# Kernel tuning notes

Measured on AMD Instinct MI355X. Metric: run time of the kernel, lower is better.

The kernel has to match this reference:

```python
import jax, jax.numpy as jnp
import numpy as np

B, S, D, H, F, NL, V = 4, 2048, 512, 8, 2048, 4, 32000
DH = D // H
EPS = 1e-6
LN_EPS = 1e-5


def _xavier(k, shape):
    lim = (6.0 / (shape[-2] + shape[-1])) ** 0.5
    return jax.random.uniform(k, shape, jnp.float32, -lim, lim)


def setup_inputs() -> dict:
    key = jax.random.key(0)
    ks = jax.random.split(key, 12)
    x = jax.random.randint(ks[0], (B, S), 0, V)
    emb = jax.random.normal(ks[1], (V, D), jnp.float32) * 0.02
    # sinusoidal positional encoding
    pos = np.arange(S, dtype=np.float32)[:, None]
    div = np.exp(np.arange(0, D, 2, dtype=np.float32) * (-np.log(10000.0) / D))
    pe_np = np.zeros((S, D), np.float32)
    pe_np[:, 0::2] = np.sin(pos * div)
    pe_np[:, 1::2] = np.cos(pos * div)
    pe = jnp.asarray(pe_np)
    return {
        "x": x, "emb": emb, "pe": pe,
        "Wq": _xavier(ks[2], (NL, D, D)), "bq": jnp.zeros((NL, D)),
        "Wk": _xavier(ks[3], (NL, D, D)), "bk": jnp.zeros((NL, D)),
        "Wv": _xavier(ks[4], (NL, D, D)), "bv": jnp.zeros((NL, D)),
        "Wo": _xavier(ks[5], (NL, D, D)), "bo": jnp.zeros((NL, D)),
        "W1": _xavier(ks[6], (NL, D, F)), "b1": jnp.zeros((NL, F)),
        "W2": _xavier(ks[7], (NL, F, D)), "b2": jnp.zeros((NL, D)),
        "g1": jnp.ones((NL, D)), "be1": jnp.zeros((NL, D)),
        "g2": jnp.ones((NL, D)), "be2": jnp.zeros((NL, D)),
        "gf": jnp.ones((D,)), "bf": jnp.zeros((D,)),
    }


def _layer_norm(h, g, b):
    mu = jnp.mean(h, axis=-1, keepdims=True)
    var = jnp.mean((h - mu) ** 2, axis=-1, keepdims=True)
    return (h - mu) * jax.lax.rsqrt(var + LN_EPS) * g + b


def _phi(u):
    # elu(x) + 1 feature map of fast-transformers causal-linear attention
    return jax.nn.elu(u) + 1.0


def _causal_linear_attention(q, k, v, key_mask):
    # q, k, v: [B, S, H, DH]; key_mask: [B, S] (1 for valid keys)
    Q = _phi(q)
    K = _phi(k) * key_mask[:, :, None, None]
    # cumulative state sum_{j<=i} K_j outer V_j : [B, S, H, DH, DH]
    St = jnp.cumsum(K[..., :, None] * v[..., None, :], axis=1)
    num = jnp.einsum("bshd,bshde->bshe", Q, St)
    Z = 1.0 / (jnp.einsum("bshd,bshd->bsh", Q, jnp.cumsum(K, axis=1)) + EPS)
    return num * Z[..., None]


def reference(x, emb, pe, Wq, bq, Wk, bk, Wv, bv, Wo, bo,
              W1, b1, W2, b2, g1, be1, g2, be2, gf, bf):
    # length mask from nonzero token count (LengthMask semantics)
    lengths = jnp.sum(jnp.abs(x) != 0, axis=-1)  # [B]
    key_mask = (jnp.arange(S)[None, :] < lengths[:, None]).astype(jnp.float32)
    h = emb[x] + pe[None, :, :]  # [B, S, D]
    for i in range(NL):
        q = (h @ Wq[i] + bq[i]).reshape(B, S, H, DH)
        k = (h @ Wk[i] + bk[i]).reshape(B, S, H, DH)
        v = (h @ Wv[i] + bv[i]).reshape(B, S, H, DH)
        a = _causal_linear_attention(q, k, v, key_mask).reshape(B, S, D)
        a = a @ Wo[i] + bo[i]
        h = _layer_norm(h + a, g1[i], be1[i])
        y = jax.nn.relu(h @ W1[i] + b1[i]) @ W2[i] + b2[i]
        h = _layer_norm(h + y, g2[i], be2[i])
    return _layer_norm(h, gf, bf)
```

## Files before the change

kernel.cpp:

```cpp
#include <hip/hip_runtime.h>
#include <math.h>

#define NLAYER 4
#define BB 4
#define SS 2048
#define DD 512
#define HH 8
#define DH 64
#define FF 2048
#define TT (BB*SS)
#define LCH 64
#define NCH (SS/LCH)
#define LN_EPS 1e-5f
#define ATT_EPS 1e-6f

typedef __bf16 bf16x8 __attribute__((ext_vector_type(8)));
typedef float  f32x4  __attribute__((ext_vector_type(4)));
typedef float  f32x16 __attribute__((ext_vector_type(16)));

__device__ __forceinline__ unsigned short f2bf(float f) {
    union { float f; unsigned u; } a; a.f = f;
    unsigned u = a.u;
    unsigned r = (u + 0x7FFFu + ((u >> 16) & 1u)) >> 16;
    return (unsigned short)r;
}
__device__ __forceinline__ float bf2f(unsigned short s) {
    union { unsigned u; float f; } a; a.u = ((unsigned)s) << 16;
    return a.f;
}
__device__ __forceinline__ float phi_f(float u) {
    return u > 0.f ? u + 1.f : __expf(u);
}

__global__ __launch_bounds__(64)
void len_kernel(const int* __restrict__ x, int* __restrict__ len) {
    const int b = blockIdx.x;
    int cnt = 0;
    for (int s = threadIdx.x; s < SS; s += 64) cnt += (x[b * SS + s] != 0);
    #pragma unroll
    for (int off = 32; off; off >>= 1) cnt += __shfl_xor(cnt, off);
    if (threadIdx.x == 0) len[b] = cnt;
}

__global__ __launch_bounds__(256)
void embed_kernel(const int* __restrict__ x, const float* __restrict__ emb,
                  const float* __restrict__ pe, unsigned short* __restrict__ h) {
    int t = blockIdx.x * 256 + threadIdx.x;
    int row = t >> 6, q = t & 63;
    int tok = x[row];
    int s = row & (SS - 1);
    const float4* ep = (const float4*)(emb + (size_t)tok * DD);
    const float4* pp = (const float4*)(pe + (size_t)s * DD);
    float4 e0 = ep[q * 2], e1 = ep[q * 2 + 1];
    float4 p0 = pp[q * 2], p1 = pp[q * 2 + 1];
    ushort4 u0 = make_ushort4(f2bf(e0.x + p0.x), f2bf(e0.y + p0.y),
                              f2bf(e0.z + p0.z), f2bf(e0.w + p0.w));
    ushort4 u1 = make_ushort4(f2bf(e1.x + p1.x), f2bf(e1.y + p1.y),
                              f2bf(e1.z + p1.z), f2bf(e1.w + p1.w));
    size_t base = (size_t)row * DD + q * 8;
    *(ushort4*)(h + base) = u0;
    *(ushort4*)(h + base + 4) = u1;
}

__global__ __launch_bounds__(256)
void transpose_cvt(const float* __restrict__ src, unsigned short* __restrict__ dst,
                   int R, int C, size_t srcLS, size_t dstLS) {
    __shared__ float tile[32][33];
    const int z = blockIdx.z;
    src += (size_t)z * srcLS;
    dst += (size_t)z * dstLS;
    const int c0 = blockIdx.x * 32, r0 = blockIdx.y * 32;
    const int tx = threadIdx.x & 31, ty = threadIdx.x >> 5;
    #pragma unroll
    for (int i = 0; i < 32; i += 8)
        tile[ty + i][tx] = src[(size_t)(r0 + ty + i) * C + c0 + tx];
    __syncthreads();
    #pragma unroll
    for (int i = 0; i < 32; i += 8)
        dst[(size_t)(c0 + ty + i) * R + r0 + tx] = f2bf(tile[tx][ty + i]);
}

__global__ __launch_bounds__(256)
void bias_concat(const float* __restrict__ bq, const float* __restrict__ bk,
                 const float* __restrict__ bv, float* __restrict__ bqkv) {
    int idx = blockIdx.x * 256 + threadIdx.x;
    if (idx >= NLAYER * 1536) return;
    int l = idx / 1536, n = idx % 1536;
    float v = n < 512 ? bq[l * 512 + n] : (n < 1024 ? bk[l * 512 + n - 512] : bv[l * 512 + n - 1024]);
    bqkv[idx] = v;
}

__device__ __forceinline__ void gll16(void* lds_ptr, const void* g_ptr) {
    __builtin_amdgcn_global_load_lds(
        (const __attribute__((address_space(1))) void*)g_ptr,
        (__attribute__((address_space(3))) void*)lds_ptr, 16, 0, 0);
}

template<int RELU, int WB>
__global__ __launch_bounds__(256, 2)
void gemm_bt(const unsigned short* __restrict__ A, const unsigned short* __restrict__ Bt,
             const float* __restrict__ bias, float* __restrict__ Cf,
             unsigned short* __restrict__ Cb, int M, int N, int K) {
    __shared__ __align__(16) char lds[2 * 2 * 128 * 64 * 2];
    const int Nt = N >> 7;
    const int bid = blockIdx.x;
    const int swz = (bid & 7) * ((int)gridDim.x >> 3) + (bid >> 3);
    const int m0 = (swz / Nt) * 128;
    const int n0 = (swz % Nt) * 128;
    const int tid = threadIdx.x;
    const int w = tid >> 6, lane = tid & 63;
    const int wr = w >> 1, wc = w & 1;
    const int srow = lane >> 3, scc = lane & 7;
    const int l32 = lane & 31, khalf = lane >> 5;

    f32x16 acc[2][2] = {};

    auto stage = [&](int buf, int k0) {
        char* base = lds + buf * 32768;
        #pragma unroll
        for (int op = 0; op < 2; ++op) {
            const unsigned short* G = op ? Bt : A;
            const int r0 = op ? n0 : m0;
            char* obase = base + op * 16384;
            #pragma unroll
            for (int i = 0; i < 4; ++i) {
                int ii = w * 4 + i;
                int row = ii * 8 + srow;
                int chunk = scc ^ (row & 7);
                gll16(obase + ii * 1024,
                      G + (size_t)(r0 + row) * K + k0 + chunk * 8);
            }
        }
    };

    stage(0, 0);
    const int nt = K >> 6;
    int buf = 0;
    const int rA = wr * 64 + l32;
    const int rB = wc * 64 + l32;

    for (int kt = 0; kt < nt; ++kt) {
        __syncthreads();
        if (kt + 1 < nt) stage(buf ^ 1, (kt + 1) << 6);
        const char* pA = lds + buf * 32768;
        const char* pB = pA + 16384;
        bf16x8 af[2][4], bfr[2][4];
        #pragma unroll
        for (int mf = 0; mf < 2; ++mf)
            #pragma unroll
            for (int kk = 0; kk < 4; ++kk) {
                int row = rA + mf * 32;
                int c = (kk * 2 + khalf) ^ (row & 7);
                af[mf][kk] = *(const bf16x8*)(pA + row * 128 + c * 16);
            }
        #pragma unroll
        for (int nf = 0; nf < 2; ++nf)
            #pragma unroll
            for (int kk = 0; kk < 4; ++kk) {
                int row = rB + nf * 32;
                int c = (kk * 2 + khalf) ^ (row & 7);
                bfr[nf][kk] = *(const bf16x8*)(pB + row * 128 + c * 16);
            }
        #pragma unroll
        for (int kk = 0; kk < 4; ++kk)
            #pragma unroll
            for (int mf = 0; mf < 2; ++mf)
                #pragma unroll
                for (int nf = 0; nf < 2; ++nf)
                    acc[mf][nf] = __builtin_amdgcn_mfma_f32_32x32x16_bf16(
                        af[mf][kk], bfr[nf][kk], acc[mf][nf], 0, 0, 0);
        buf ^= 1;
    }

    #pragma unroll
    for (int nf = 0; nf < 2; ++nf) {
        int col = n0 + wc * 64 + nf * 32 + l32;
        float bi = bias[col];
        #pragma unroll
        for (int mf = 0; mf < 2; ++mf) {
            int rowb = m0 + wr * 64 + mf * 32 + 4 * khalf;
            #pragma unroll
            for (int reg = 0; reg < 16; ++reg) {
                int row = rowb + (reg & 3) + 8 * (reg >> 2);
                float v = acc[mf][nf][reg] + bi;
                if (RELU) v = v > 0.f ? v : 0.f;
                if (WB) Cb[(size_t)row * N + col] = f2bf(v);
                else    Cf[(size_t)row * N + col] = v;
            }
        }
    }
}

template<int RELU>
__global__ __launch_bounds__(512, 2)
void gemm_big(const unsigned short* __restrict__ A, const unsigned short* __restrict__ Bt,
              const float* __restrict__ bias, unsigned short* __restrict__ Cb,
              int M, int N, int K) {
    __shared__ __align__(16) char lds[3 * 49152];
    const int Nt = N >> 7;
    const int bid = blockIdx.x;
    const int swz = (bid & 7) * ((int)gridDim.x >> 3) + (bid >> 3);
    const int m0 = (swz / Nt) * 256;
    const int n0 = (swz % Nt) * 128;
    const int tid = threadIdx.x;
    const int w = tid >> 6, lane = tid & 63;
    const int wr = w >> 1, wc = w & 1;
    const int l32 = lane & 31, khalf = lane >> 5;

    f32x16 acc[2][2] = {};

    auto stage = [&](int buf, int k0) {
        char* base = lds + buf * 49152;
        #pragma unroll
        for (int s = 0; s < 4; ++s) {
            int lin0 = s * 512 + w * 64;
            int lin = lin0 + lane;
            int row = lin >> 3, chunk = lin & 7;
            gll16(base + lin0 * 16,
                  A + (size_t)(m0 + row) * K + k0 + ((chunk ^ (row & 7)) << 3));
        }
        #pragma unroll
        for (int s = 0; s < 2; ++s) {
            int lin0 = s * 512 + w * 64;
            int lin = lin0 + lane;
            int row = lin >> 3, chunk = lin & 7;
            gll16(base + 32768 + lin0 * 16,
                  Bt + (size_t)(n0 + row) * K + k0 + ((chunk ^ (row & 7)) << 3));
        }
    };

    const int nt = K >> 6;
    stage(0, 0);
    stage(1, 64);
    int cur = 0;
    const int rA = wr * 64 + l32;
    const int rB = wc * 64 + l32;

    for (int t = 0; t < nt; ++t) {
        asm volatile("s_waitcnt lgkmcnt(0)" ::: "memory");
        if (t + 1 < nt) asm volatile("s_waitcnt vmcnt(6)" ::: "memory");
        else            asm volatile("s_waitcnt vmcnt(0)" ::: "memory");
        __builtin_amdgcn_s_barrier();
        __builtin_amdgcn_sched_barrier(0);
        if (t + 2 < nt) {
            int nb = cur + 2; if (nb >= 3) nb -= 3;
            stage(nb, (t + 2) << 6);
        }
        const char* pA = lds + cur * 49152;
        const char* pB = pA + 32768;
        bf16x8 af[2][4], bfr[2][4];
        #pragma unroll
        for (int mf = 0; mf < 2; ++mf)
            #pragma unroll
            for (int kk = 0; kk < 4; ++kk) {
                int row = rA + mf * 32;
                int c = (kk * 2 + khalf) ^ (row & 7);
                af[mf][kk] = *(const bf16x8*)(pA + row * 128 + c * 16);
            }
        #pragma unroll
        for (int nf = 0; nf < 2; ++nf)
            #pragma unroll
            for (int kk = 0; kk < 4; ++kk) {
                int row = rB + nf * 32;
                int c = (kk * 2 + khalf) ^ (row & 7);
                bfr[nf][kk] = *(const bf16x8*)(pB + row * 128 + c * 16);
            }
        #pragma unroll
        for (int kk = 0; kk < 4; ++kk)
            #pragma unroll
            for (int mf = 0; mf < 2; ++mf)
                #pragma unroll
                for (int nf = 0; nf < 2; ++nf)
                    acc[mf][nf] = __builtin_amdgcn_mfma_f32_32x32x16_bf16(
                        af[mf][kk], bfr[nf][kk], acc[mf][nf], 0, 0, 0);
        cur = (cur + 1 == 3) ? 0 : cur + 1;
    }

    #pragma unroll
    for (int nf = 0; nf < 2; ++nf) {
        int col = n0 + wc * 64 + nf * 32 + l32;
        float bi = bias[col];
        #pragma unroll
        for (int mf = 0; mf < 2; ++mf) {
            int rowb = m0 + wr * 64 + mf * 32 + 4 * khalf;
            #pragma unroll
            for (int reg = 0; reg < 16; ++reg) {
                int row = rowb + (reg & 3) + 8 * (reg >> 2);
                float v = acc[mf][nf][reg] + bi;
                if (RELU) v = v > 0.f ? v : 0.f;
                Cb[(size_t)row * N + col] = f2bf(v);
            }
        }
    }
}

__global__ __launch_bounds__(256)
void attn_chunk_sums(const unsigned short* __restrict__ qkv, const int* __restrict__ len,
                     unsigned short* __restrict__ states, float* __restrict__ ksum) {
    const int c = blockIdx.x & (NCH - 1);
    const int bh = blockIdx.x / NCH;
    const int b = bh >> 3, h = bh & 7;
    const int L = len[b];
    const int tid = threadIdx.x;
    const int w = tid >> 6, lane = tid & 63;
    __shared__ __align__(16) unsigned short Kt[64 * 64];
    __shared__ __align__(16) unsigned short Vt[64 * 64];
    __shared__ float ksumP[4][64];

    float kpart = 0.f;
    #pragma unroll 8
    for (int t = 0; t < 16; ++t) {
        const int jj = 4 * t + w;
        const int d = lane;
        const int sglob = c * 64 + jj;
        const unsigned short* base = qkv + (size_t)(b * SS + sglob) * 1536 + h * 64 + d;
        float kv = bf2f(base[512]);
        float kp = (sglob < L) ? phi_f(kv) : 0.f;
        kpart += kp;
        const int sw = (((jj >> 3) ^ (d & 7)) << 3) + (jj & 7);
        Kt[d * 64 + sw] = f2bf(kp);
        Vt[d * 64 + sw] = base[1024];
    }
    ksumP[w][lane] = kpart;
    __syncthreads();

    const int frow = w * 16 + (lane & 15);
    const int g = lane >> 4;
    bf16x8 ak[2];
    #pragma unroll
    for (int kk = 0; kk < 2; ++kk)
        ak[kk] = *(const bf16x8*)&Kt[frow * 64 + (((kk * 4 + g) ^ (frow & 7)) << 3)];
    f32x4 oc[4] = {};
    #pragma unroll
    for (int ef = 0; ef < 4; ++ef) {
        int brow = ef * 16 + (lane & 15);
        #pragma unroll
        for (int kk = 0; kk < 2; ++kk) {
            bf16x8 bv = *(const bf16x8*)&Vt[brow * 64 + (((kk * 4 + g) ^ (brow & 7)) << 3)];
            oc[ef] = __builtin_amdgcn_mfma_f32_16x16x32_bf16(ak[kk], bv, oc[ef], 0, 0, 0);
        }
    }
    unsigned short* so = states + (size_t)blockIdx.x * 4096;
    #pragma unroll
    for (int ef = 0; ef < 4; ++ef)
        #pragma unroll
        for (int r = 0; r < 4; ++r) {
            int dd = w * 16 + g * 4 + r;
            int e = ef * 16 + (lane & 15);
            so[dd * 64 + e] = f2bf(oc[ef][r]);
        }
    if (w == 0) {
        float s = ksumP[0][lane] + ksumP[1][lane] + ksumP[2][lane] + ksumP[3][lane];
        ksum[(size_t)blockIdx.x * 64 + lane] = s;
    }
}

__global__ __launch_bounds__(256)
void attn_prefix(const unsigned short* __restrict__ states, const float* __restrict__ ksum,
                 unsigned short* __restrict__ sprefix, float* __restrict__ kprefix) {
    const int bh = blockIdx.x >> 4;
    const int idx = (blockIdx.x & 15) * 256 + threadIdx.x;
    size_t base = (size_t)bh * NCH * 4096 + idx;
    float run = 0.f;
    #pragma unroll 4
    for (int cc = 0; cc < NCH; ++cc) {
        size_t o = base + (size_t)cc * 4096;
        float v = bf2f(states[o]);
        sprefix[o] = f2bf(run);
        run += v;
    }
    if ((blockIdx.x & 15) == 0 && threadIdx.x < 64) {
        size_t kb = (size_t)bh * NCH * 64 + threadIdx.x;
        float krun = 0.f;
        for (int cc = 0; cc < NCH; ++cc) {
            size_t o = kb + (size_t)cc * 64;
            float v = ksum[o];
            kprefix[o] = krun;
            krun += v;
        }
    }
}

__global__ __launch_bounds__(256)
void attn_output(const unsigned short* __restrict__ qkv, const int* __restrict__ len,
                 const unsigned short* __restrict__ sprefix, const float* __restrict__ kprefix,
                 unsigned short* __restrict__ a_bf) {
    const int c = blockIdx.x & (NCH - 1);
    const int bh = blockIdx.x / NCH;
    const int b = bh >> 3, h = bh & 7;
    const int L = len[b];
    const int tid = threadIdx.x;
    const int w = tid >> 6, lane = tid & 63;

    __shared__ __align__(16) unsigned short Qb[64 * 64];
    __shared__ __align__(16) unsigned short Kb[64 * 64];
    __shared__ __align__(16) unsigned short SpT[64 * 64];
    __shared__ __align__(16) unsigned short Vt[64 * 64];
    __shared__ __align__(16) unsigned short Amb[64 * 64];
    __shared__ float zq[64];
    __shared__ float zinv[64];

    const float kspv = kprefix[(size_t)(bh * NCH + c) * 64 + lane];
    const unsigned short* Sp = sprefix + (size_t)(bh * NCH + c) * 4096;

    #pragma unroll 4
    for (int t = 0; t < 16; ++t) {
        const int jj = 4 * t + w;
        const int d = lane;
        const int sglob = c * 64 + jj;
        const unsigned short* base = qkv + (size_t)(b * SS + sglob) * 1536 + h * 64 + d;
        float qv = bf2f(base[0]), kv = bf2f(base[512]);
        float qp = phi_f(qv);
        float kp = (sglob < L) ? phi_f(kv) : 0.f;
        const int swr = (((d >> 3) ^ (jj & 7)) << 3) + (d & 7);
        Qb[jj * 64 + swr] = f2bf(qp);
        Kb[jj * 64 + swr] = f2bf(kp);
        const int swt = (((jj >> 3) ^ (d & 7)) << 3) + (jj & 7);
        Vt[d * 64 + swt] = base[1024];
        SpT[d * 64 + swt] = Sp[jj * 64 + d];
        float zc = qp * kspv;
        #pragma unroll
        for (int off = 32; off; off >>= 1) zc += __shfl_xor(zc, off);
        if (lane == 0) zq[jj] = zc;
    }
    __syncthreads();

    const int frow = w * 16 + (lane & 15);
    const int g = lane >> 4;
    bf16x8 aq[2];
    #pragma unroll
    for (int kk = 0; kk < 2; ++kk)
        aq[kk] = *(const bf16x8*)&Qb[frow * 64 + (((kk * 4 + g) ^ (frow & 7)) << 3)];

    f32x4 am[4] = {};
    #pragma unroll
    for (int jf = 0; jf < 4; ++jf) {
        int brow = jf * 16 + (lane & 15);
        #pragma unroll
        for (int kk = 0; kk < 2; ++kk) {
            bf16x8 bk = *(const bf16x8*)&Kb[brow * 64 + (((kk * 4 + g) ^ (brow & 7)) << 3)];
            am[jf] = __builtin_amdgcn_mfma_f32_16x16x32_bf16(aq[kk], bk, am[jf], 0, 0, 0);
        }
    }

    float zl[4] = {0.f, 0.f, 0.f, 0.f};
    #pragma unroll
    for (int jf = 0; jf < 4; ++jf) {
        #pragma unroll
        for (int r = 0; r < 4; ++r) {
            int i = w * 16 + g * 4 + r;
            int j = jf * 16 + (lane & 15);
            float v = (j <= i) ? am[jf][r] : 0.f;
            zl[r] += v;
            Amb[i * 64 + (((j >> 3) ^ (i & 7)) << 3) + (j & 7)] = f2bf(v);
        }
    }
    #pragma unroll
    for (int r = 0; r < 4; ++r)
        #pragma unroll
        for (int off = 1; off < 16; off <<= 1) zl[r] += __shfl_xor(zl[r], off);
    #pragma unroll
    for (int r = 0; r < 4; ++r) {
        if ((lane & 15) == r) {
            int i = w * 16 + g * 4 + r;
            zinv[i] = 1.f / (zl[r] + zq[i] + ATT_EPS);
        }
    }

    f32x4 oc[4] = {};
    #pragma unroll
    for (int ef = 0; ef < 4; ++ef) {
        int brow = ef * 16 + (lane & 15);
        #pragma unroll
        for (int kk = 0; kk < 2; ++kk) {
            bf16x8 bs = *(const bf16x8*)&SpT[brow * 64 + (((kk * 4 + g) ^ (brow & 7)) << 3)];
            oc[ef] = __builtin_amdgcn_mfma_f32_16x16x32_bf16(aq[kk], bs, oc[ef], 0, 0, 0);
        }
    }
    bf16x8 aam[2];
    #pragma unroll
    for (int kk = 0; kk < 2; ++kk)
        aam[kk] = *(const bf16x8*)&Amb[frow * 64 + (((kk * 4 + g) ^ (frow & 7)) << 3)];
    #pragma unroll
    for (int ef = 0; ef < 4; ++ef) {
        int brow = ef * 16 + (lane & 15);
        #pragma unroll
        for (int kk = 0; kk < 2; ++kk) {
            bf16x8 bv = *(const bf16x8*)&Vt[brow * 64 + (((kk * 4 + g) ^ (brow & 7)) << 3)];
            oc[ef] = __builtin_amdgcn_mfma_f32_16x16x32_bf16(aam[kk], bv, oc[ef], 0, 0, 0);
        }
    }

    __syncthreads();
    #pragma unroll
    for (int ef = 0; ef < 4; ++ef) {
        #pragma unroll
        for (int r = 0; r < 4; ++r) {
            int i = w * 16 + g * 4 + r;
            int e = ef * 16 + (lane & 15);
            float zi = zinv[i];
            Kb[i * 64 + (((e >> 3) ^ (i & 7)) << 3) + (e & 7)] = f2bf(oc[ef][r] * zi);
        }
    }
    __syncthreads();
    {
        unsigned short* dst = a_bf + (size_t)(b * SS + c * 64) * 512 + h * 64;
        #pragma unroll
        for (int u = 0; u < 2; ++u) {
            int cid = tid + u * 256;
            int row = cid >> 3, cb = cid & 7;
            int4 val = *(const int4*)&Kb[row * 64 + ((cb ^ (row & 7)) << 3)];
            *(int4*)(dst + (size_t)row * 512 + cb * 8) = val;
        }
    }
}

template<int ADD, int FINAL>
__global__ __launch_bounds__(256)
void ln_kernel(const unsigned short* __restrict__ hin, const unsigned short* __restrict__ add,
               const float* __restrict__ gw, const float* __restrict__ bw,
               unsigned short* __restrict__ hout, float* __restrict__ fout) {
    const int row = blockIdx.x * 4 + (threadIdx.x >> 6);
    const int lane = threadIdx.x & 63;
    const size_t base = (size_t)row * DD + lane * 8;
    float v[8];
    {
        ushort4 a0 = *(const ushort4*)(hin + base);
        ushort4 a1 = *(const ushort4*)(hin + base + 4);
        v[0] = bf2f(a0.x); v[1] = bf2f(a0.y); v[2] = bf2f(a0.z); v[3] = bf2f(a0.w);
        v[4] = bf2f(a1.x); v[5] = bf2f(a1.y); v[6] = bf2f(a1.z); v[7] = bf2f(a1.w);
    }
    if (ADD) {
        ushort4 b0 = *(const ushort4*)(add + base);
        ushort4 b1 = *(const ushort4*)(add + base + 4);
        v[0] += bf2f(b0.x); v[1] += bf2f(b0.y); v[2] += bf2f(b0.z); v[3] += bf2f(b0.w);
        v[4] += bf2f(b1.x); v[5] += bf2f(b1.y); v[6] += bf2f(b1.z); v[7] += bf2f(b1.w);
    }
    float s = 0.f;
    #pragma unroll
    for (int i = 0; i < 8; ++i) s += v[i];
    #pragma unroll
    for (int off = 32; off; off >>= 1) s += __shfl_xor(s, off);
    float mu = s * (1.f / 512.f);
    float sq = 0.f;
    #pragma unroll
    for (int i = 0; i < 8; ++i) { float d = v[i] - mu; sq += d * d; }
    #pragma unroll
    for (int off = 32; off; off >>= 1) sq += __shfl_xor(sq, off);
    float rs = 1.f / sqrtf(sq * (1.f / 512.f) + LN_EPS);
    float4 g0 = ((const float4*)gw)[lane * 2], g1v = ((const float4*)gw)[lane * 2 + 1];
    float4 b0 = ((const float4*)bw)[lane * 2], b1v = ((const float4*)bw)[lane * 2 + 1];
    float gg[8] = {g0.x, g0.y, g0.z, g0.w, g1v.x, g1v.y, g1v.z, g1v.w};
    float bb[8] = {b0.x, b0.y, b0.z, b0.w, b1v.x, b1v.y, b1v.z, b1v.w};
    float o[8];
    #pragma unroll
    for (int i = 0; i < 8; ++i) o[i] = (v[i] - mu) * rs * gg[i] + bb[i];
    if (FINAL) {
        *(float4*)(fout + base)     = make_float4(o[0], o[1], o[2], o[3]);
        *(float4*)(fout + base + 4) = make_float4(o[4], o[5], o[6], o[7]);
    } else {
        *(ushort4*)(hout + base)     = make_ushort4(f2bf(o[0]), f2bf(o[1]), f2bf(o[2]), f2bf(o[3]));
        *(ushort4*)(hout + base + 4) = make_ushort4(f2bf(o[4]), f2bf(o[5]), f2bf(o[6]), f2bf(o[7]));
    }
}

extern "C" void kernel_launch(void* const* d_in, const int* in_sizes, int n_in,
                              void* d_out, int out_size, void* d_ws, size_t ws_size,
                              hipStream_t stream) {
    (void)in_sizes; (void)n_in; (void)out_size; (void)ws_size;
    const int*   x   = (const int*)d_in[0];
    const float* emb = (const float*)d_in[1];
    const float* pe  = (const float*)d_in[2];
    const float* Wq  = (const float*)d_in[3];
    const float* bq  = (const float*)d_in[4];
    const float* Wk  = (const float*)d_in[5];
    const float* bk  = (const float*)d_in[6];
    const float* Wv  = (const float*)d_in[7];
    const float* bv  = (const float*)d_in[8];
    const float* Wo  = (const float*)d_in[9];
    const float* bo  = (const float*)d_in[10];
    const float* W1  = (const float*)d_in[11];
    const float* b1  = (const float*)d_in[12];
    const float* W2  = (const float*)d_in[13];
    const float* b2  = (const float*)d_in[14];
    const float* g1  = (const float*)d_in[15];
    const float* be1 = (const float*)d_in[16];
    const float* g2  = (const float*)d_in[17];
    const float* be2 = (const float*)d_in[18];
    const float* gf  = (const float*)d_in[19];
    const float* bff = (const float*)d_in[20];
    float* out = (float*)d_out;

    char* ws = (char*)d_ws;
    size_t off = 0;
    auto alloc = [&](size_t bytes) -> void* {
        void* p = ws + off; off += (bytes + 255) & ~(size_t)255; return p;
    };
    int* len              = (int*)alloc(16);
    unsigned short* qkv_t = (unsigned short*)alloc((size_t)NLAYER * 1536 * 512 * 2);
    unsigned short* wo_t  = (unsigned short*)alloc((size_t)NLAYER * 512 * 512 * 2);
    unsigned short* w1_t  = (unsigned short*)alloc((size_t)NLAYER * 2048 * 512 * 2);
    unsigned short* w2_t  = (unsigned short*)alloc((size_t)NLAYER * 512 * 2048 * 2);
    float* bqkv           = (float*)alloc((size_t)NLAYER * 1536 * 4);
    unsigned short* h     = (unsigned short*)alloc((size_t)TT * 512 * 2);
    unsigned short* qkv   = (unsigned short*)alloc((size_t)TT * 1536 * 2);
    unsigned short* a_bf  = (unsigned short*)alloc((size_t)TT * 512 * 2);
    unsigned short* obuf  = (unsigned short*)alloc((size_t)TT * 512 * 2);
    unsigned short* y1_bf = (unsigned short*)alloc((size_t)TT * 2048 * 2);
    unsigned short* states  = (unsigned short*)alloc((size_t)32 * NCH * 4096 * 2);
    float* ksum           = (float*)alloc((size_t)32 * NCH * 64 * 4);
    unsigned short* sprefix = (unsigned short*)alloc((size_t)32 * NCH * 4096 * 2);
    float* kprefix        = (float*)alloc((size_t)32 * NCH * 64 * 4);

    len_kernel<<<BB, 64, 0, stream>>>(x, len);
    embed_kernel<<<(TT * 64) / 256, 256, 0, stream>>>(x, emb, pe, h);

    dim3 tb(256);
    transpose_cvt<<<dim3(16, 16, NLAYER), tb, 0, stream>>>(Wq, qkv_t,             512, 512, (size_t)512*512, (size_t)1536*512);
    transpose_cvt<<<dim3(16, 16, NLAYER), tb, 0, stream>>>(Wk, qkv_t + 512*512,   512, 512, (size_t)512*512, (size_t)1536*512);
    transpose_cvt<<<dim3(16, 16, NLAYER), tb, 0, stream>>>(Wv, qkv_t + 1024*512,  512, 512, (size_t)512*512, (size_t)1536*512);
    transpose_cvt<<<dim3(16, 16, NLAYER), tb, 0, stream>>>(Wo, wo_t,              512, 512, (size_t)512*512, (size_t)512*512);
    transpose_cvt<<<dim3(64, 16, NLAYER), tb, 0, stream>>>(W1, w1_t,              512, 2048, (size_t)512*2048, (size_t)2048*512);
    transpose_cvt<<<dim3(16, 64, NLAYER), tb, 0, stream>>>(W2, w2_t,              2048, 512, (size_t)2048*512, (size_t)512*2048);
    bias_concat<<<(NLAYER * 1536 + 255) / 256, 256, 0, stream>>>(bq, bk, bv, bqkv);

    for (int l = 0; l < NLAYER; ++l) {
        gemm_big<0><<<(TT/256) * (1536/128), 512, 0, stream>>>(
            h, qkv_t + (size_t)l*1536*512, bqkv + l*1536, qkv, TT, 1536, 512);
        attn_chunk_sums<<<32 * NCH, 256, 0, stream>>>(qkv, len, states, ksum);
        attn_prefix<<<32 * 16, 256, 0, stream>>>(states, ksum, sprefix, kprefix);
        attn_output<<<32 * NCH, 256, 0, stream>>>(qkv, len, sprefix, kprefix, a_bf);
        gemm_bt<0,1><<<(TT/128) * (512/128), 256, 0, stream>>>(
            a_bf, wo_t + (size_t)l*512*512, bo + l*512, nullptr, obuf, TT, 512, 512);
        ln_kernel<1,0><<<TT/4, 256, 0, stream>>>(h, obuf, g1 + l*512, be1 + l*512, h, nullptr);
        gemm_big<1><<<(TT/256) * (2048/128), 512, 0, stream>>>(
            h, w1_t + (size_t)l*2048*512, b1 + l*2048, y1_bf, TT, 2048, 512);
        gemm_bt<0,1><<<(TT/128) * (512/128), 256, 0, stream>>>(
            y1_bf, w2_t + (size_t)l*512*2048, b2 + l*512, nullptr, obuf, TT, 512, 2048);
        ln_kernel<1,0><<<TT/4, 256, 0, stream>>>(h, obuf, g2 + l*512, be2 + l*512, h, nullptr);
    }
    ln_kernel<0,1><<<TT/4, 256, 0, stream>>>(h, nullptr, gf, bff, nullptr, out);
}
```

Measured before the change: 569.9 us.

## Replace triple-buffered 256x128 GEMM with single-buffer 128x128 tile kernel

The QKV and FFN1 GEMMs move from a 512-thread, 256x128-tile kernel with a three-stage async LDS pipeline to a 256-thread, 128x128-tile kernel. The new kernel uses a single 32KB LDS buffer and synchronises around each K step. The smaller LDS footprint and tiles allow more resident blocks and more blocks in the grid, aiming for higher occupancy. In exchange it loses the prefetch overlap between global loads and MFMA work and gets less operand reuse per tile.

```diff
diff --git a/kernel.cpp b/kernel.cpp
--- a/kernel.cpp
+++ b/kernel.cpp
@@ -192,62 +192,50 @@
 }
 
 template<int RELU>
-__global__ __launch_bounds__(512, 2)
-void gemm_big(const unsigned short* __restrict__ A, const unsigned short* __restrict__ Bt,
-              const float* __restrict__ bias, unsigned short* __restrict__ Cb,
-              int M, int N, int K) {
-    __shared__ __align__(16) char lds[3 * 49152];
+__global__ __launch_bounds__(256, 3)
+void gemm_sb(const unsigned short* __restrict__ A, const unsigned short* __restrict__ Bt,
+             const float* __restrict__ bias, unsigned short* __restrict__ Cb,
+             int M, int N, int K) {
+    __shared__ __align__(16) char lds[2 * 128 * 64 * 2];
     const int Nt = N >> 7;
     const int bid = blockIdx.x;
     const int swz = (bid & 7) * ((int)gridDim.x >> 3) + (bid >> 3);
-    const int m0 = (swz / Nt) * 256;
+    const int m0 = (swz / Nt) * 128;
     const int n0 = (swz % Nt) * 128;
     const int tid = threadIdx.x;
     const int w = tid >> 6, lane = tid & 63;
     const int wr = w >> 1, wc = w & 1;
+    const int srow = lane >> 3, scc = lane & 7;
     const int l32 = lane & 31, khalf = lane >> 5;
 
     f32x16 acc[2][2] = {};
 
-    auto stage = [&](int buf, int k0) {
-        char* base = lds + buf * 49152;
-        #pragma unroll
-        for (int s = 0; s < 4; ++s) {
-            int lin0 = s * 512 + w * 64;
-            int lin = lin0 + lane;
-            int row = lin >> 3, chunk = lin & 7;
-            gll16(base + lin0 * 16,
-                  A + (size_t)(m0 + row) * K + k0 + ((chunk ^ (row & 7)) << 3));
-        }
-        #pragma unroll
-        for (int s = 0; s < 2; ++s) {
-            int lin0 = s * 512 + w * 64;
-            int lin = lin0 + lane;
-            int row = lin >> 3, chunk = lin & 7;
-            gll16(base + 32768 + lin0 * 16,
-                  Bt + (size_t)(n0 + row) * K + k0 + ((chunk ^ (row & 7)) << 3));
+    auto stage = [&](int k0) {
+        #pragma unroll
+        for (int op = 0; op < 2; ++op) {
+            const unsigned short* G = op ? Bt : A;
+            const int r0 = op ? n0 : m0;
+            char* obase = lds + op * 16384;
+            #pragma unroll
+            for (int i = 0; i < 4; ++i) {
+                int ii = w * 4 + i;
+                int row = ii * 8 + srow;
+                int chunk = scc ^ (row & 7);
+                gll16(obase + ii * 1024,
+                      G + (size_t)(r0 + row) * K + k0 + chunk * 8);
+            }
         }
     };
 
     const int nt = K >> 6;
-    stage(0, 0);
-    stage(1, 64);
-    int cur = 0;
     const int rA = wr * 64 + l32;
     const int rB = wc * 64 + l32;
 
-    for (int t = 0; t < nt; ++t) {
-        asm volatile("s_waitcnt lgkmcnt(0)" ::: "memory");
-        if (t + 1 < nt) asm volatile("s_waitcnt vmcnt(6)" ::: "memory");
-        else            asm volatile("s_waitcnt vmcnt(0)" ::: "memory");
-        __builtin_amdgcn_s_barrier();
-        __builtin_amdgcn_sched_barrier(0);
-        if (t + 2 < nt) {
-            int nb = cur + 2; if (nb >= 3) nb -= 3;
-            stage(nb, (t + 2) << 6);
-        }
-        const char* pA = lds + cur * 49152;
-        const char* pB = pA + 32768;
+    for (int kt = 0; kt < nt; ++kt) {
+        stage(kt << 6);
+        __syncthreads();
+        const char* pA = lds;
+        const char* pB = pA + 16384;
         bf16x8 af[2][4], bfr[2][4];
         #pragma unroll
         for (int mf = 0; mf < 2; ++mf)
@@ -273,7 +261,7 @@
                 for (int nf = 0; nf < 2; ++nf)
                     acc[mf][nf] = __builtin_amdgcn_mfma_f32_32x32x16_bf16(
                         af[mf][kk], bfr[nf][kk], acc[mf][nf], 0, 0, 0);
-        cur = (cur + 1 == 3) ? 0 : cur + 1;
+        if (kt + 1 < nt) __syncthreads();
     }
 
     #pragma unroll
@@ -625,7 +613,7 @@
     bias_concat<<<(NLAYER * 1536 + 255) / 256, 256, 0, stream>>>(bq, bk, bv, bqkv);
 
     for (int l = 0; l < NLAYER; ++l) {
-        gemm_big<0><<<(TT/256) * (1536/128), 512, 0, stream>>>(
+        gemm_sb<0><<<(TT/128) * (1536/128), 256, 0, stream>>>(
             h, qkv_t + (size_t)l*1536*512, bqkv + l*1536, qkv, TT, 1536, 512);
         attn_chunk_sums<<<32 * NCH, 256, 0, stream>>>(qkv, len, states, ksum);
         attn_prefix<<<32 * 16, 256, 0, stream>>>(states, ksum, sprefix, kprefix);
@@ -633,7 +621,7 @@
         gemm_bt<0,1><<<(TT/128) * (512/128), 256, 0, stream>>>(
             a_bf, wo_t + (size_t)l*512*512, bo + l*512, nullptr, obuf, TT, 512, 512);
         ln_kernel<1,0><<<TT/4, 256, 0, stream>>>(h, obuf, g1 + l*512, be1 + l*512, h, nullptr);
-        gemm_big<1><<<(TT/256) * (2048/128), 512, 0, stream>>>(
+        gemm_sb<1><<<(TT/128) * (2048/128), 256, 0, stream>>>(
             h, w1_t + (size_t)l*2048*512, b1 + l*2048, y1_bf, TT, 2048, 512);
         gemm_bt<0,1><<<(TT/128) * (512/128), 256, 0, stream>>>(
             y1_bf, w2_t + (size_t)l*512*2048, b2 + l*512, nullptr, obuf, TT, 512, 2048);
```

Result: faster. 554.5 us (-2.7%).
